# Kernel optimization log

Hardware: AMD Instinct MI355X
Metric: run time of the kernel (lower is better)

Reference implementation:

```python
import jax, jax.numpy as jnp
import numpy as np

D_MODEL = 1024
H = 16
D_K = D_MODEL // H


def setup_inputs() -> dict:
    key = jax.random.key(0)
    ks = jax.random.split(key, 7)
    B, S = 4, 2048
    scale = 1.0 / np.sqrt(D_MODEL)
    return {
        "q": jax.random.normal(ks[0], (B, S, D_MODEL), dtype=jnp.float32),
        "k": jax.random.normal(ks[1], (B, S, D_MODEL), dtype=jnp.float32),
        "v": jax.random.normal(ks[2], (B, S, D_MODEL), dtype=jnp.float32),
        "W_q": jax.random.normal(ks[3], (D_MODEL, D_MODEL), dtype=jnp.float32) * scale,
        "W_k": jax.random.normal(ks[4], (D_MODEL, D_MODEL), dtype=jnp.float32) * scale,
        "W_v": jax.random.normal(ks[5], (D_MODEL, D_MODEL), dtype=jnp.float32) * scale,
        "W_o": jax.random.normal(ks[6], (D_MODEL, D_MODEL), dtype=jnp.float32) * scale,
    }


def reference(q, k, v, W_q, W_k, W_v, W_o):
    B, S, _ = q.shape
    # nn.Linear(bias=False): y = x @ W.T
    def proj(x, W):
        return (x @ W.T).reshape(B, -1, H, D_K).transpose(0, 2, 1, 3)  # [B,H,S,d_k]
    Q = proj(q, W_q)
    K = proj(k, W_k)
    V = proj(v, W_v)
    scores = jnp.einsum('bhqd,bhkd->bhqk', Q, K) / jnp.sqrt(jnp.float32(D_K))
    attn = jax.nn.softmax(scores, axis=-1)  # dropout p=0.0 -> identity
    ctx = jnp.einsum('bhqk,bhkd->bhqd', attn, V)
    ctx = ctx.transpose(0, 2, 1, 3).reshape(B, S, H * D_K)
    return ctx @ W_o.T
```

## Files before the change

### kernel.cpp

```cpp
#include <hip/hip_runtime.h>
#include <stdint.h>


typedef __attribute__((ext_vector_type(8))) short bf16x8;
typedef __attribute__((ext_vector_type(4))) short bf16x4;
typedef __attribute__((ext_vector_type(4))) float f32x4;

__device__ __forceinline__ void lds_async16(const void* g, void* l) {
  __builtin_amdgcn_global_load_lds(
      (const __attribute__((address_space(1))) void*)g,
      (__attribute__((address_space(3))) void*)l, 16, 0, 0);
}

__device__ __forceinline__ unsigned short f2bf(float f) {
  union { float f; unsigned u; } v; v.f = f;
  unsigned u = v.u + 0x7fffu + ((v.u >> 16) & 1u);
  return (unsigned short)(u >> 16);
}

__device__ __forceinline__ float fast_exp2(float x) {
#if __has_builtin(__builtin_amdgcn_exp2f)
  return __builtin_amdgcn_exp2f(x);
#else
  return exp2f(x);
#endif
}

__device__ __forceinline__ unsigned pk2(float a, float b) {
#if __has_builtin(__builtin_amdgcn_cvt_pk_bf16_f32)
  typedef __bf16 bf16v2 __attribute__((ext_vector_type(2)));
  union { bf16v2 v; unsigned u; } x;
  x.v = __builtin_amdgcn_cvt_pk_bf16_f32(a, b);
  return x.u;
#else
  return (unsigned)f2bf(a) | ((unsigned)f2bf(b) << 16);
#endif
}

__global__ void cvt_kernel(const float* s0, const float* s1, const float* s2, const float* s3,
                           unsigned short* d0, unsigned short* d1, unsigned short* d2, unsigned short* d3,
                           int n4) {
  int which = blockIdx.y;
  const float* s = which == 0 ? s0 : which == 1 ? s1 : which == 2 ? s2 : s3;
  unsigned short* d = which == 0 ? d0 : which == 1 ? d1 : which == 2 ? d2 : d3;
  int i = blockIdx.x * 256 + threadIdx.x;
  if (i < n4) {
    float4 v = ((const float4*)s)[i];
    ushort4 o;
    o.x = f2bf(v.x); o.y = f2bf(v.y); o.z = f2bf(v.z); o.w = f2bf(v.w);
    ((ushort4*)d)[i] = o;
  }
}

struct GemmAcc { f32x4 acc[4][4]; };

__device__ __forceinline__ void gemm_core(const unsigned short* __restrict__ Arows,
                                          const unsigned short* __restrict__ Brows,
                                          int tm, int tn, unsigned short* As,
                                          unsigned short* Bs, GemmAcc& g) {
  constexpr int K = 1024;
  const int tid = threadIdx.x;
  const int lane = tid & 63;
  const int wv = tid >> 6;
  const int wm = wv & 1, wn = wv >> 1;
  const int c16 = lane & 15, q4 = lane >> 4;

#pragma unroll
  for (int i = 0; i < 4; ++i)
#pragma unroll
    for (int j = 0; j < 4; ++j)
#pragma unroll
      for (int r = 0; r < 4; ++r) g.acc[i][j][r] = 0.f;

  const int srow = tid >> 3;
  const int gc = (((tid & 7) ^ (srow & 7)) << 3);
  const unsigned short* Arow = Arows + (size_t)(tm * 128 + srow) * K + gc;
  const unsigned short* Brow = Brows + (size_t)(tn * 128 + srow) * K + gc;
  char* AsBase = (char*)As + tid * 16;
  char* BsBase = (char*)Bs + tid * 16;

  for (int k0 = 0; k0 < K; k0 += 64) {
    __syncthreads();
#pragma unroll
    for (int i = 0; i < 4; ++i) {
      lds_async16(Arow + k0 + i * 32 * K, AsBase + i * 4096);
      lds_async16(Brow + k0 + i * 32 * K, BsBase + i * 4096);
    }
    __syncthreads();
#pragma unroll
    for (int ks = 0; ks < 2; ++ks) {
      bf16x8 af[4], bfr[4];
#pragma unroll
      for (int i = 0; i < 4; ++i) {
        int mr = wm * 64 + i * 16 + c16;
        int pa = (ks * 4 + q4) ^ (mr & 7);
        af[i] = *(const bf16x8*)(As + mr * 64 + pa * 8);
        int nr = wn * 64 + i * 16 + c16;
        int pb = (ks * 4 + q4) ^ (nr & 7);
        bfr[i] = *(const bf16x8*)(Bs + nr * 64 + pb * 8);
      }
#pragma unroll
      for (int i = 0; i < 4; ++i)
#pragma unroll
        for (int j = 0; j < 4; ++j)
          g.acc[i][j] = __builtin_amdgcn_mfma_f32_16x16x32_bf16(af[i], bfr[j], g.acc[i][j], 0, 0, 0);
    }
  }
}

__global__ __launch_bounds__(256, 2)
void qkv_kernel(const unsigned short* __restrict__ qb, const unsigned short* __restrict__ kb,
                const unsigned short* __restrict__ vb,
                const unsigned short* __restrict__ wq, const unsigned short* __restrict__ wk,
                const unsigned short* __restrict__ wv_,
                unsigned short* __restrict__ Qb, unsigned short* __restrict__ Kb,
                unsigned short* __restrict__ Vtb) {
  __shared__ unsigned short As[128 * 64];
  __shared__ unsigned short Bs[128 * 64];
  const int z = blockIdx.z;
  const unsigned short* A;
  const unsigned short* B;
  int tm, tn;
  if (z == 0)      { A = qb;  B = wq;  tm = blockIdx.y; tn = blockIdx.x; }
  else if (z == 1) { A = kb;  B = wk;  tm = blockIdx.y; tn = blockIdx.x; }
  else             { A = wv_; B = vb;  tm = blockIdx.x; tn = blockIdx.y; }

  GemmAcc g;
  gemm_core(A, B, tm, tn, As, Bs, g);

  const int lane = threadIdx.x & 63;
  const int wv = threadIdx.x >> 6;
  const int wm = wv & 1, wn = wv >> 1;
  const int c16 = lane & 15, q4 = lane >> 4;
  const float qscale = 0.125f * 1.44269504f;

#pragma unroll
  for (int i = 0; i < 4; ++i)
#pragma unroll
    for (int j = 0; j < 4; ++j)
#pragma unroll
      for (int r = 0; r < 4; ++r) {
        int m = tm * 128 + wm * 64 + i * 16 + q4 * 4 + r;
        int n = tn * 128 + wn * 64 + j * 16 + c16;
        float val = g.acc[i][j][r];
        if (z < 2) {
          if (z == 0) val *= qscale;
          int b = m >> 11, s_ = m & 2047, h = n >> 6, d = n & 63;
          unsigned short* dst = z == 0 ? Qb : Kb;
          dst[(((size_t)(b * 16 + h) * 2048 + s_) << 6) | d] = f2bf(val);
        } else {
          int h = m >> 6, d = m & 63, b = n >> 11, s_ = n & 2047;
          Vtb[((size_t)((b * 16 + h) * 64 + d) << 11) | s_] = f2bf(val);
        }
      }
}

__global__ __launch_bounds__(256, 2)
void out_gemm(const unsigned short* __restrict__ A, const unsigned short* __restrict__ B,
              float* __restrict__ C) {
  __shared__ unsigned short As[128 * 64];
  __shared__ unsigned short Bs[128 * 64];
  GemmAcc g;
  gemm_core(A, B, blockIdx.y, blockIdx.x, As, Bs, g);
  const int lane = threadIdx.x & 63;
  const int wv = threadIdx.x >> 6;
  const int wm = wv & 1, wn = wv >> 1;
  const int c16 = lane & 15, q4 = lane >> 4;
#pragma unroll
  for (int i = 0; i < 4; ++i)
#pragma unroll
    for (int j = 0; j < 4; ++j)
#pragma unroll
      for (int r = 0; r < 4; ++r) {
        int m = blockIdx.y * 128 + wm * 64 + i * 16 + q4 * 4 + r;
        int n = blockIdx.x * 128 + wn * 64 + j * 16 + c16;
        C[(size_t)m * 1024 + n] = g.acc[i][j][r];
      }
}

__global__ __launch_bounds__(256, 4)
void attn_kernel(const unsigned short* __restrict__ Q,
                 const unsigned short* __restrict__ K,
                 const unsigned short* __restrict__ Vt,
                 unsigned short* __restrict__ ctx) {
  __shared__ unsigned short Ks[128 * 64];
  __shared__ unsigned short Vs[64 * 128];

  const int tid = threadIdx.x, lane = tid & 63, w = tid >> 6;
  const int c16 = lane & 15, q4 = lane >> 4;
  const int wbase = w * 32;
  const int bh = blockIdx.y, qt = blockIdx.x;
  const unsigned short* Qp = Q + ((size_t)bh * 2048 + qt * 128) * 64;
  const unsigned short* Kp = K + (size_t)bh * 2048 * 64;
  const unsigned short* Vp = Vt + (size_t)bh * 64 * 2048;

  const int srow8 = tid >> 3;
  const int gc8 = (((tid & 7) ^ (srow8 & 7)) << 3);

  {
    const unsigned short* Qr = Qp + (size_t)srow8 * 64 + gc8;
    char* base = (char*)Ks + tid * 16;
#pragma unroll
    for (int c = 0; c < 4; ++c) lds_async16(Qr + c * 32 * 64, base + c * 4096);
  }
  __syncthreads();
  bf16x8 qf[2][2];
#pragma unroll
  for (int nn = 0; nn < 2; ++nn)
#pragma unroll
    for (int ks = 0; ks < 2; ++ks) {
      int qr = wbase + nn * 16 + c16;
      int pos = (ks * 4 + q4) ^ (qr & 7);
      qf[nn][ks] = *(const bf16x8*)(Ks + qr * 64 + pos * 8);
    }

  bf16x8 onesf;
  {
    short v = (c16 == 0) ? (short)0x3F80 : (short)0;
#pragma unroll
    for (int j = 0; j < 8; ++j) onesf[j] = v;
  }

  f32x4 oacc[2][4];
  f32x4 lacc[2];
#pragma unroll
  for (int mm = 0; mm < 2; ++mm) {
#pragma unroll
    for (int r = 0; r < 4; ++r) lacc[mm][r] = 0.f;
#pragma unroll
    for (int dj = 0; dj < 4; ++dj)
#pragma unroll
      for (int r = 0; r < 4; ++r) oacc[mm][dj][r] = 0.f;
  }

  const int vrow = tid >> 4;
  const int vslot = tid & 15;
  const int vchunk = vslot ^ (vrow & 15);

  for (int kt = 0; kt < 16; ++kt) {
    __syncthreads();
    {
      const unsigned short* Kr = Kp + ((size_t)kt * 128 + srow8) * 64 + gc8;
      char* base = (char*)Ks + tid * 16;
#pragma unroll
      for (int c = 0; c < 4; ++c) lds_async16(Kr + c * 32 * 64, base + c * 4096);
    }
    {
      const unsigned short* Vr = Vp + (size_t)vrow * 2048 + kt * 128 + vchunk * 8;
      char* base = (char*)Vs + tid * 16;
#pragma unroll
      for (int c = 0; c < 4; ++c) lds_async16(Vr + (size_t)c * 16 * 2048, base + c * 4096);
    }
    __syncthreads();

#pragma unroll
    for (int ks2 = 0; ks2 < 4; ++ks2) {
      f32x4 s[2][2];
#pragma unroll
      for (int ms = 0; ms < 2; ++ms) {
        const int row = (ks2 * 2 + ms) * 16 + c16;
        const bf16x8 kf0 = *(const bf16x8*)(Ks + row * 64 + ((0 + q4) ^ (row & 7)) * 8);
        const bf16x8 kf1 = *(const bf16x8*)(Ks + row * 64 + ((4 + q4) ^ (row & 7)) * 8);
        f32x4 z0 = {0.f, 0.f, 0.f, 0.f}, z1 = {0.f, 0.f, 0.f, 0.f};
        z0 = __builtin_amdgcn_mfma_f32_16x16x32_bf16(kf0, qf[0][0], z0, 0, 0, 0);
        z0 = __builtin_amdgcn_mfma_f32_16x16x32_bf16(kf1, qf[0][1], z0, 0, 0, 0);
        z1 = __builtin_amdgcn_mfma_f32_16x16x32_bf16(kf0, qf[1][0], z1, 0, 0, 0);
        z1 = __builtin_amdgcn_mfma_f32_16x16x32_bf16(kf1, qf[1][1], z1, 0, 0, 0);
        s[ms][0] = z0;
        s[ms][1] = z1;
      }
      union PU { unsigned u[4]; bf16x8 v; };
      PU pf0, pf1;
#pragma unroll
      for (int ms = 0; ms < 2; ++ms) {
        pf0.u[ms * 2]     = pk2(fast_exp2(s[ms][0][0]), fast_exp2(s[ms][0][1]));
        pf0.u[ms * 2 + 1] = pk2(fast_exp2(s[ms][0][2]), fast_exp2(s[ms][0][3]));
        pf1.u[ms * 2]     = pk2(fast_exp2(s[ms][1][0]), fast_exp2(s[ms][1][1]));
        pf1.u[ms * 2 + 1] = pk2(fast_exp2(s[ms][1][2]), fast_exp2(s[ms][1][3]));
      }
      lacc[0] = __builtin_amdgcn_mfma_f32_16x16x32_bf16(pf0.v, onesf, lacc[0], 0, 0, 0);
      lacc[1] = __builtin_amdgcn_mfma_f32_16x16x32_bf16(pf1.v, onesf, lacc[1], 0, 0, 0);
      const int cb = ks2 * 4 + (q4 >> 1);
      const int co = (q4 & 1) * 4;
#pragma unroll
      for (int dj = 0; dj < 4; ++dj) {
        const int dr = dj * 16 + c16;
        union VU { bf16x4 h[2]; bf16x8 v; } vf;
        vf.h[0] = *(const bf16x4*)(Vs + dr * 128 + ((cb) ^ (dr & 15)) * 8 + co);
        vf.h[1] = *(const bf16x4*)(Vs + dr * 128 + ((cb + 2) ^ (dr & 15)) * 8 + co);
        oacc[0][dj] = __builtin_amdgcn_mfma_f32_16x16x32_bf16(pf0.v, vf.v, oacc[0][dj], 0, 0, 0);
        oacc[1][dj] = __builtin_amdgcn_mfma_f32_16x16x32_bf16(pf1.v, vf.v, oacc[1][dj], 0, 0, 0);
      }
    }
  }

  int b = bh >> 4, h = bh & 15;
#pragma unroll
  for (int mm = 0; mm < 2; ++mm)
#pragma unroll
    for (int r = 0; r < 4; ++r) {
      float l = __shfl(lacc[mm][r], lane & 48, 64);
      float inv = 1.f / l;
      int s_ = qt * 128 + wbase + mm * 16 + q4 * 4 + r;
#pragma unroll
      for (int dj = 0; dj < 4; ++dj) {
        int d = dj * 16 + c16;
        ctx[((size_t)(b * 2048 + s_)) * 1024 + h * 64 + d] = f2bf(oacc[mm][dj][r] * inv);
      }
    }
}

extern "C" void kernel_launch(void* const* d_in, const int* in_sizes, int n_in,
                              void* d_out, int out_size, void* d_ws, size_t ws_size,
                              hipStream_t stream) {
  const float* q  = (const float*)d_in[0];
  const float* k  = (const float*)d_in[1];
  const float* v  = (const float*)d_in[2];
  const float* Wq = (const float*)d_in[3];
  const float* Wk = (const float*)d_in[4];
  const float* Wv = (const float*)d_in[5];
  const float* Wo = (const float*)d_in[6];

  char* ws = (char*)d_ws;
  unsigned short* qb  = (unsigned short*)(ws);
  unsigned short* kb  = (unsigned short*)(ws + (16u << 20));
  unsigned short* vb  = (unsigned short*)(ws + (32u << 20));
  unsigned short* wqb = (unsigned short*)(ws + (48u << 20));
  unsigned short* wkb = (unsigned short*)(ws + (50u << 20));
  unsigned short* wvb = (unsigned short*)(ws + (52u << 20));
  unsigned short* wob = (unsigned short*)(ws + (54u << 20));
  unsigned short* Qb  = (unsigned short*)(ws + (56u << 20));
  unsigned short* Kb  = (unsigned short*)(ws + (72u << 20));
  unsigned short* Vtb = (unsigned short*)(ws + (88u << 20));
  unsigned short* ctxb = qb;

  cvt_kernel<<<dim3(1024, 4), 256, 0, stream>>>(Wq, Wk, Wv, Wo, wqb, wkb, wvb, wob, 262144);
  cvt_kernel<<<dim3(8192, 3), 256, 0, stream>>>(q, k, v, q, qb, kb, vb, qb, 2097152);

  qkv_kernel<<<dim3(8, 64, 3), 256, 0, stream>>>(qb, kb, vb, wqb, wkb, wvb, Qb, Kb, Vtb);

  attn_kernel<<<dim3(16, 64), 256, 0, stream>>>(Qb, Kb, Vtb, ctxb);

  out_gemm<<<dim3(8, 64), 256, 0, stream>>>(ctxb, wob, (float*)d_out);
}
```

Baseline: 329.4 us.

## Double-buffer K/V tiles, widen attention query tile, permute V layout

The attention kernel now handles 256 queries per block (64 per wave), so each K/V tile loaded into LDS is reused across twice as many queries. K and V tiles are double-buffered, with the next tile's async loads issued before computing on the current one, which removes one barrier per iteration. The V-transpose store in the QKV kernel permutes the sequence index within each 128-chunk so a single 16-byte LDS read yields the PV operand instead of two 8-byte reads. The cost is more registers and LDS per block, lower occupancy (launch bounds 4 to 2), and half as many blocks in the grid.

```diff
diff --git a/kernel.cpp b/kernel.cpp
--- a/kernel.cpp
+++ b/kernel.cpp
@@ -3,7 +3,6 @@
 
 
 typedef __attribute__((ext_vector_type(8))) short bf16x8;
-typedef __attribute__((ext_vector_type(4))) short bf16x4;
 typedef __attribute__((ext_vector_type(4))) float f32x4;
 
 __device__ __forceinline__ void lds_async16(const void* g, void* l) {
@@ -150,6 +149,9 @@
           dst[(((size_t)(b * 16 + h) * 2048 + s_) << 6) | d] = f2bf(val);
         } else {
           int h = m >> 6, d = m & 63, b = n >> 11, s_ = n & 2047;
+          int sl = s_ & 127;
+          int sp = (sl & ~31) | (((sl >> 2) & 3) << 3) | (((sl >> 4) & 1) << 2) | (sl & 3);
+          s_ = (s_ & ~127) | sp;
           Vtb[((size_t)((b * 16 + h) * 64 + d) << 11) | s_] = f2bf(val);
         }
       }
@@ -178,19 +180,19 @@
       }
 }
 
-__global__ __launch_bounds__(256, 4)
+__global__ __launch_bounds__(256, 2)
 void attn_kernel(const unsigned short* __restrict__ Q,
                  const unsigned short* __restrict__ K,
                  const unsigned short* __restrict__ Vt,
                  unsigned short* __restrict__ ctx) {
-  __shared__ unsigned short Ks[128 * 64];
-  __shared__ unsigned short Vs[64 * 128];
+  __shared__ unsigned short Ks[2][128 * 64];
+  __shared__ unsigned short Vs[2][64 * 128];
 
   const int tid = threadIdx.x, lane = tid & 63, w = tid >> 6;
   const int c16 = lane & 15, q4 = lane >> 4;
-  const int wbase = w * 32;
+  const int wbase = w * 64;
   const int bh = blockIdx.y, qt = blockIdx.x;
-  const unsigned short* Qp = Q + ((size_t)bh * 2048 + qt * 128) * 64;
+  const unsigned short* Qp = Q + ((size_t)bh * 2048 + qt * 256) * 64;
   const unsigned short* Kp = K + (size_t)bh * 2048 * 64;
   const unsigned short* Vp = Vt + (size_t)bh * 64 * 2048;
 
@@ -201,18 +203,20 @@
     const unsigned short* Qr = Qp + (size_t)srow8 * 64 + gc8;
     char* base = (char*)Ks + tid * 16;
 #pragma unroll
-    for (int c = 0; c < 4; ++c) lds_async16(Qr + c * 32 * 64, base + c * 4096);
+    for (int c = 0; c < 8; ++c) lds_async16(Qr + c * 32 * 64, base + c * 4096);
   }
   __syncthreads();
-  bf16x8 qf[2][2];
-#pragma unroll
-  for (int nn = 0; nn < 2; ++nn)
+  const unsigned short* Kflat = &Ks[0][0];
+  bf16x8 qf[4][2];
+#pragma unroll
+  for (int nn = 0; nn < 4; ++nn)
 #pragma unroll
     for (int ks = 0; ks < 2; ++ks) {
       int qr = wbase + nn * 16 + c16;
       int pos = (ks * 4 + q4) ^ (qr & 7);
-      qf[nn][ks] = *(const bf16x8*)(Ks + qr * 64 + pos * 8);
-    }
+      qf[nn][ks] = *(const bf16x8*)(Kflat + qr * 64 + pos * 8);
+    }
+  __syncthreads();
 
   bf16x8 onesf;
   {
@@ -221,91 +225,103 @@
     for (int j = 0; j < 8; ++j) onesf[j] = v;
   }
 
-  f32x4 oacc[2][4];
-  f32x4 lacc[2];
-#pragma unroll
-  for (int mm = 0; mm < 2; ++mm) {
-#pragma unroll
-    for (int r = 0; r < 4; ++r) lacc[mm][r] = 0.f;
+  f32x4 oacc[4][4];
+  f32x4 lacc[4];
+#pragma unroll
+  for (int nn = 0; nn < 4; ++nn) {
+#pragma unroll
+    for (int r = 0; r < 4; ++r) lacc[nn][r] = 0.f;
 #pragma unroll
     for (int dj = 0; dj < 4; ++dj)
 #pragma unroll
-      for (int r = 0; r < 4; ++r) oacc[mm][dj][r] = 0.f;
+      for (int r = 0; r < 4; ++r) oacc[nn][dj][r] = 0.f;
   }
 
   const int vrow = tid >> 4;
   const int vslot = tid & 15;
   const int vchunk = vslot ^ (vrow & 15);
-
+  const unsigned short* Kr0 = Kp + (size_t)srow8 * 64 + gc8;
+  const unsigned short* Vr0 = Vp + (size_t)vrow * 2048 + vchunk * 8;
+
+  {
+    char* kb = (char*)Ks[0] + tid * 16;
+    char* vb = (char*)Vs[0] + tid * 16;
+#pragma unroll
+    for (int c = 0; c < 4; ++c) {
+      lds_async16(Kr0 + c * 32 * 64, kb + c * 4096);
+      lds_async16(Vr0 + (size_t)c * 16 * 2048, vb + c * 4096);
+    }
+  }
+
+  int cur = 0;
   for (int kt = 0; kt < 16; ++kt) {
     __syncthreads();
-    {
-      const unsigned short* Kr = Kp + ((size_t)kt * 128 + srow8) * 64 + gc8;
-      char* base = (char*)Ks + tid * 16;
-#pragma unroll
-      for (int c = 0; c < 4; ++c) lds_async16(Kr + c * 32 * 64, base + c * 4096);
-    }
-    {
-      const unsigned short* Vr = Vp + (size_t)vrow * 2048 + kt * 128 + vchunk * 8;
-      char* base = (char*)Vs + tid * 16;
-#pragma unroll
-      for (int c = 0; c < 4; ++c) lds_async16(Vr + (size_t)c * 16 * 2048, base + c * 4096);
-    }
-    __syncthreads();
+    if (kt < 15) {
+      char* kb = (char*)Ks[cur ^ 1] + tid * 16;
+      char* vb = (char*)Vs[cur ^ 1] + tid * 16;
+      const unsigned short* Krn = Kr0 + (size_t)(kt + 1) * 128 * 64;
+      const unsigned short* Vrn = Vr0 + (size_t)(kt + 1) * 128;
+#pragma unroll
+      for (int c = 0; c < 4; ++c) {
+        lds_async16(Krn + c * 32 * 64, kb + c * 4096);
+        lds_async16(Vrn + (size_t)c * 16 * 2048, vb + c * 4096);
+      }
+    }
+
+    const unsigned short* KsC = Ks[cur];
+    const unsigned short* VsC = Vs[cur];
 
 #pragma unroll
     for (int ks2 = 0; ks2 < 4; ++ks2) {
-      f32x4 s[2][2];
+      f32x4 s[2][4];
 #pragma unroll
       for (int ms = 0; ms < 2; ++ms) {
         const int row = (ks2 * 2 + ms) * 16 + c16;
-        const bf16x8 kf0 = *(const bf16x8*)(Ks + row * 64 + ((0 + q4) ^ (row & 7)) * 8);
-        const bf16x8 kf1 = *(const bf16x8*)(Ks + row * 64 + ((4 + q4) ^ (row & 7)) * 8);
-        f32x4 z0 = {0.f, 0.f, 0.f, 0.f}, z1 = {0.f, 0.f, 0.f, 0.f};
-        z0 = __builtin_amdgcn_mfma_f32_16x16x32_bf16(kf0, qf[0][0], z0, 0, 0, 0);
-        z0 = __builtin_amdgcn_mfma_f32_16x16x32_bf16(kf1, qf[0][1], z0, 0, 0, 0);
-        z1 = __builtin_amdgcn_mfma_f32_16x16x32_bf16(kf0, qf[1][0], z1, 0, 0, 0);
-        z1 = __builtin_amdgcn_mfma_f32_16x16x32_bf16(kf1, qf[1][1], z1, 0, 0, 0);
-        s[ms][0] = z0;
-        s[ms][1] = z1;
-      }
-      union PU { unsigned u[4]; bf16x8 v; };
-      PU pf0, pf1;
-#pragma unroll
-      for (int ms = 0; ms < 2; ++ms) {
-        pf0.u[ms * 2]     = pk2(fast_exp2(s[ms][0][0]), fast_exp2(s[ms][0][1]));
-        pf0.u[ms * 2 + 1] = pk2(fast_exp2(s[ms][0][2]), fast_exp2(s[ms][0][3]));
-        pf1.u[ms * 2]     = pk2(fast_exp2(s[ms][1][0]), fast_exp2(s[ms][1][1]));
-        pf1.u[ms * 2 + 1] = pk2(fast_exp2(s[ms][1][2]), fast_exp2(s[ms][1][3]));
-      }
-      lacc[0] = __builtin_amdgcn_mfma_f32_16x16x32_bf16(pf0.v, onesf, lacc[0], 0, 0, 0);
-      lacc[1] = __builtin_amdgcn_mfma_f32_16x16x32_bf16(pf1.v, onesf, lacc[1], 0, 0, 0);
-      const int cb = ks2 * 4 + (q4 >> 1);
-      const int co = (q4 & 1) * 4;
+        const bf16x8 kf0 = *(const bf16x8*)(KsC + row * 64 + ((0 + q4) ^ (row & 7)) * 8);
+        const bf16x8 kf1 = *(const bf16x8*)(KsC + row * 64 + ((4 + q4) ^ (row & 7)) * 8);
+#pragma unroll
+        for (int nn = 0; nn < 4; ++nn) {
+          f32x4 z = {0.f, 0.f, 0.f, 0.f};
+          z = __builtin_amdgcn_mfma_f32_16x16x32_bf16(kf0, qf[nn][0], z, 0, 0, 0);
+          z = __builtin_amdgcn_mfma_f32_16x16x32_bf16(kf1, qf[nn][1], z, 0, 0, 0);
+          s[ms][nn] = z;
+        }
+      }
+      bf16x8 pfv[4];
+#pragma unroll
+      for (int nn = 0; nn < 4; ++nn) {
+        union PU { unsigned u[4]; bf16x8 v; } pf;
+        pf.u[0] = pk2(fast_exp2(s[0][nn][0]), fast_exp2(s[0][nn][1]));
+        pf.u[1] = pk2(fast_exp2(s[0][nn][2]), fast_exp2(s[0][nn][3]));
+        pf.u[2] = pk2(fast_exp2(s[1][nn][0]), fast_exp2(s[1][nn][1]));
+        pf.u[3] = pk2(fast_exp2(s[1][nn][2]), fast_exp2(s[1][nn][3]));
+        pfv[nn] = pf.v;
+        lacc[nn] = __builtin_amdgcn_mfma_f32_16x16x32_bf16(pf.v, onesf, lacc[nn], 0, 0, 0);
+      }
 #pragma unroll
       for (int dj = 0; dj < 4; ++dj) {
         const int dr = dj * 16 + c16;
-        union VU { bf16x4 h[2]; bf16x8 v; } vf;
-        vf.h[0] = *(const bf16x4*)(Vs + dr * 128 + ((cb) ^ (dr & 15)) * 8 + co);
-        vf.h[1] = *(const bf16x4*)(Vs + dr * 128 + ((cb + 2) ^ (dr & 15)) * 8 + co);
-        oacc[0][dj] = __builtin_amdgcn_mfma_f32_16x16x32_bf16(pf0.v, vf.v, oacc[0][dj], 0, 0, 0);
-        oacc[1][dj] = __builtin_amdgcn_mfma_f32_16x16x32_bf16(pf1.v, vf.v, oacc[1][dj], 0, 0, 0);
-      }
-    }
+        const bf16x8 vf = *(const bf16x8*)(VsC + dr * 128 + (((ks2 * 4 + q4) ^ (dr & 15))) * 8);
+#pragma unroll
+        for (int nn = 0; nn < 4; ++nn)
+          oacc[nn][dj] = __builtin_amdgcn_mfma_f32_16x16x32_bf16(pfv[nn], vf, oacc[nn][dj], 0, 0, 0);
+      }
+    }
+    cur ^= 1;
   }
 
   int b = bh >> 4, h = bh & 15;
 #pragma unroll
-  for (int mm = 0; mm < 2; ++mm)
+  for (int nn = 0; nn < 4; ++nn)
 #pragma unroll
     for (int r = 0; r < 4; ++r) {
-      float l = __shfl(lacc[mm][r], lane & 48, 64);
+      float l = __shfl(lacc[nn][r], lane & 48, 64);
       float inv = 1.f / l;
-      int s_ = qt * 128 + wbase + mm * 16 + q4 * 4 + r;
+      int s_ = qt * 256 + wbase + nn * 16 + q4 * 4 + r;
 #pragma unroll
       for (int dj = 0; dj < 4; ++dj) {
         int d = dj * 16 + c16;
-        ctx[((size_t)(b * 2048 + s_)) * 1024 + h * 64 + d] = f2bf(oacc[mm][dj][r] * inv);
+        ctx[((size_t)(b * 2048 + s_)) * 1024 + h * 64 + d] = f2bf(oacc[nn][dj][r] * inv);
       }
     }
 }
@@ -339,7 +355,7 @@
 
   qkv_kernel<<<dim3(8, 64, 3), 256, 0, stream>>>(qb, kb, vb, wqb, wkb, wvb, Qb, Kb, Vtb);
 
-  attn_kernel<<<dim3(16, 64), 256, 0, stream>>>(Qb, Kb, Vtb, ctxb);
+  attn_kernel<<<dim3(8, 64), 256, 0, stream>>>(Qb, Kb, Vtb, ctxb);
 
   out_gemm<<<dim3(8, 64), 256, 0, stream>>>(ctxb, wob, (float*)d_out);
 }
```

After: 331.6 us. No clear change (+0.7%).
